# Kernel optimization log

Measured on AMD Instinct MI355X. Metric: run time of the kernel, lower is better.

## Reference

```python
import jax, jax.numpy as jnp
import numpy as np

B, N, D, K = 4, 256, 128, 8
H = 2 * D   # MLP hidden
F3 = 3 * D  # pair feature dim


def setup_inputs() -> dict:
    key = jax.random.key(0)
    ks = jax.random.split(key, 9)
    init = lambda k, shape: (jax.random.normal(k, shape, jnp.float32) * 0.02)
    s = jax.random.normal(ks[0], (B, N, D), jnp.float32)
    return {
        "s": s,
        "Wg1": init(ks[1], (F3, H)), "bg1": jnp.zeros((H,), jnp.float32),
        "Wg2": init(ks[2], (H, 1)),  "bg2": jnp.zeros((1,), jnp.float32),
        "Wa1": init(ks[3], (F3, H)), "ba1": jnp.zeros((H,), jnp.float32),
        "Wa2": init(ks[4], (H, 1)),  "ba2": jnp.zeros((1,), jnp.float32),
    }


def _mlp(x, W1, b1, W2, b2):
    # 2-layer MLP: Linear -> ReLU -> Linear (dropout inactive at eval)
    return jax.nn.relu(x @ W1 + b1) @ W2 + b2


def reference(s, Wg1, bg1, Wg2, bg2, Wa1, ba1, Wa2, ba2):
    b, n, d = s.shape
    si = s[:, :, None, :]                      # [B,N,1,D]
    sj = s[:, None, :, :]                      # [B,1,N,D]
    pair = jnp.concatenate([
        jnp.broadcast_to(si, (b, n, n, d)),
        jnp.broadcast_to(sj, (b, n, n, d)),
        si * sj,
    ], axis=-1)                                # [B,N,N,3D]

    # Stage 1: discrete top-K peer gating
    scores = _mlp(pair, Wg1, bg1, Wg2, bg2)[..., 0]   # [B,N,N]
    k = min(K, n)
    _, topk_idx = jax.lax.top_k(scores, k)            # [B,N,K]
    gate = jax.nn.one_hot(topk_idx, n, dtype=jnp.float32).sum(-2)  # [B,N,N] binary

    # Stage 2: soft relevance weighting over selected peers
    att_logits = _mlp(pair, Wa1, ba1, Wa2, ba2)[..., 0]            # [B,N,N]
    att_logits = jnp.where(gate > 0, att_logits, -jnp.inf)
    att_weights = jnp.nan_to_num(jax.nn.softmax(att_logits, axis=-1))

    ctx = jnp.einsum('bij,bij,bjd->bid', gate, att_weights, s)     # [B,N,D]
    return ctx, gate, att_weights
```

## Files before the change

kernel.cpp:

```cpp
#include <hip/hip_runtime.h>
#include <math.h>

#define B_ 4
#define N_ 256
#define D_ 128
#define H_ 256
#define K_ 8
#define NJP 64

typedef short v8s __attribute__((ext_vector_type(8)));
typedef float v16f __attribute__((ext_vector_type(16)));

__device__ inline void split_bf16(float x, unsigned short& hi, unsigned short& lo) {
  unsigned u = __float_as_uint(x);
  unsigned uh = u & 0xFFFF0000u;
  hi = (unsigned short)(uh >> 16);
  float r = x - __uint_as_float(uh);
  unsigned ur = __float_as_uint(r);
  ur += 0x7FFFu + ((ur >> 16) & 1u);
  lo = (unsigned short)(ur >> 16);
}

__global__ __launch_bounds__(256) void prep_all(
    const float* __restrict__ s,
    const float* __restrict__ Wg1, const float* __restrict__ bg1,
    const float* __restrict__ Wa1, const float* __restrict__ ba1,
    float* __restrict__ Ag, float* __restrict__ Aa,
    unsigned short* __restrict__ Wghi, unsigned short* __restrict__ Wglo,
    unsigned short* __restrict__ Wahi,
    unsigned short* __restrict__ Sfh, unsigned short* __restrict__ Sfl) {
  __shared__ float sh[D_];
  const int blk = blockIdx.x;
  if (blk < 1024) {
    const int b = blk >> 8, n = blk & 255, h = threadIdx.x;
    if (h < D_) sh[h] = s[(b * N_ + n) * D_ + h];
    __syncthreads();
    float ag = bg1[h], aa = ba1[h];
#pragma unroll 8
    for (int d = 0; d < D_; d++) {
      ag = fmaf(sh[d], Wg1[d * H_ + h], ag);
      aa = fmaf(sh[d], Wa1[d * H_ + h], aa);
    }
    Ag[(b * N_ + n) * H_ + h] = ag;
    Aa[(b * N_ + n) * H_ + h] = aa;
  } else if (blk < 1152) {
    const int id = blk - 1024;
    if (threadIdx.x < 64) {
      const int ks = id >> 3, tile = id & 7, lane = threadIdx.x;
      const int h = tile * 32 + (lane & 31);
      const int kbase = ks * 16 + (lane >> 5) * 8;
      const int idx0 = (id * 64 + lane) * 8;
#pragma unroll
      for (int e = 0; e < 8; e++) {
        const int k = kbase + e;
        const int f = (k < D_) ? (2 * D_ + k) : k;
        unsigned short x, y;
        split_bf16(Wg1[f * H_ + h], x, y);
        Wghi[idx0 + e] = x;
        Wglo[idx0 + e] = y;
        unsigned short xa, ya;
        split_bf16(Wa1[f * H_ + h], xa, ya);
        Wahi[idx0 + e] = xa;
      }
    }
  } else {
    const int id = blk - 1152;
    const int b = id >> 3, jt = id & 7;
    const int lane = threadIdx.x & 63, k0 = threadIdx.x >> 6;
    const int j = jt * 32 + (lane & 31);
#pragma unroll
    for (int ksl = k0; ksl < 8; ksl += 4) {
      const int d = ksl * 16 + (lane >> 5) * 8;
      const float* sp = s + (b * N_ + j) * D_ + d;
      const float4 f0 = *(const float4*)(sp);
      const float4 f1 = *(const float4*)(sp + 4);
      v8s vh, vl;
      unsigned short x, y;
      split_bf16(f0.x, x, y); vh[0] = (short)x; vl[0] = (short)y;
      split_bf16(f0.y, x, y); vh[1] = (short)x; vl[1] = (short)y;
      split_bf16(f0.z, x, y); vh[2] = (short)x; vl[2] = (short)y;
      split_bf16(f0.w, x, y); vh[3] = (short)x; vl[3] = (short)y;
      split_bf16(f1.x, x, y); vh[4] = (short)x; vl[4] = (short)y;
      split_bf16(f1.y, x, y); vh[5] = (short)x; vl[5] = (short)y;
      split_bf16(f1.z, x, y); vh[6] = (short)x; vl[6] = (short)y;
      split_bf16(f1.w, x, y); vh[7] = (short)x; vl[7] = (short)y;
      const int dst = (((b * 8 + jt) * 8 + ksl) * 64 + lane) * 8;
      *(v8s*)(Sfh + dst) = vh;
      *(v8s*)(Sfl + dst) = vl;
    }
  }
}

__device__ inline void arg_better(float v2, int i2, float& v, int& idx) {
  if (v2 > v || (v2 == v && i2 < idx)) { v = v2; idx = i2; }
}

__device__ inline int a_idx(int jl, int k) {
  return (((jl >> 5) * 8 + (k >> 4)) * 64 + ((k >> 3) & 1) * 32 + (jl & 31)) * 8
         + (k & 7);
}
#define ALO 8192

__global__ __launch_bounds__(256, 2) void score_kernel(
    const float* __restrict__ s,
    const float* __restrict__ Ag, const float* __restrict__ Aa,
    const unsigned short* __restrict__ Sfh, const unsigned short* __restrict__ Sfl,
    const unsigned short* __restrict__ Wghi, const unsigned short* __restrict__ Wglo,
    const unsigned short* __restrict__ Wahi,
    const float* __restrict__ Wg2, const float* __restrict__ bg2p,
    const float* __restrict__ Wa2, const float* __restrict__ ba2p,
    float* __restrict__ out) {
  const int b = blockIdx.x >> 8;
  const int i = blockIdx.x & 255;
  const int t = threadIdx.x;
  const int wv = t >> 6, lane = t & 63;
  const int m32 = lane & 31, half32 = lane >> 5;

  __shared__ __align__(16) unsigned short a_all[2 * ALO + 64];
  __shared__ float si_sh[D_];
  __shared__ float sc_part[8 * NJP];
  __shared__ float scg_sh[N_];
  __shared__ float attl_sh[N_];
  __shared__ float red_v[4];
  __shared__ int red_i[4];
  __shared__ int sel_list[K_];

  if (t < D_) si_sh[t] = s[(b * N_ + i) * D_ + t];

  float agv[2], w2g[2], aav[2], w2a[2];
#pragma unroll
  for (int ht = 0; ht < 2; ht++) {
    const int hg = wv * 64 + ht * 32 + m32;
    agv[ht] = Ag[(b * N_ + i) * H_ + hg];
    w2g[ht] = Wg2[hg];
    aav[ht] = Aa[(b * N_ + i) * H_ + hg];
    w2a[ht] = Wa2[hg];
  }

  const int boff = ((2 * wv) * 64 + lane) * 8;

#define MF(A_, B_v, C_) C_ = __builtin_amdgcn_mfma_f32_32x32x16_bf16(A_, B_v, C_, 0, 0, 0)

#pragma unroll 1
  for (int ph = 0; ph < 4; ph++) {
    __syncthreads();
    {
      const int jl = t >> 2, kq = t & 3;
      const int jg = b * N_ + ph * NJP + jl;
      const float* srow = s + jg * D_ + kq * 32;
      const float* sic = si_sh + kq * 32;
#pragma unroll
      for (int u = 0; u < 4; u++) {
        const float4 sv0 = *(const float4*)(srow + u * 8);
        const float4 sv1 = *(const float4*)(srow + u * 8 + 4);
        v8s vh, vl;
        unsigned short x, y;
        split_bf16(sic[u * 8 + 0] * sv0.x, x, y); vh[0] = (short)x; vl[0] = (short)y;
        split_bf16(sic[u * 8 + 1] * sv0.y, x, y); vh[1] = (short)x; vl[1] = (short)y;
        split_bf16(sic[u * 8 + 2] * sv0.z, x, y); vh[2] = (short)x; vl[2] = (short)y;
        split_bf16(sic[u * 8 + 3] * sv0.w, x, y); vh[3] = (short)x; vl[3] = (short)y;
        split_bf16(sic[u * 8 + 4] * sv1.x, x, y); vh[4] = (short)x; vl[4] = (short)y;
        split_bf16(sic[u * 8 + 5] * sv1.y, x, y); vh[5] = (short)x; vl[5] = (short)y;
        split_bf16(sic[u * 8 + 6] * sv1.z, x, y); vh[6] = (short)x; vl[6] = (short)y;
        split_bf16(sic[u * 8 + 7] * sv1.w, x, y); vh[7] = (short)x; vl[7] = (short)y;
        const int idx = a_idx(jl, kq * 32 + u * 8);
        *(v8s*)(a_all + idx) = vh;
        *(v8s*)(a_all + ALO + idx) = vl;
      }
    }
    __syncthreads();

    const unsigned short* sf_base_h = Sfh + ((b * 8 + ph * 2) * 8) * 512 + lane * 8;
    const unsigned short* sf_base_l = Sfl + ((b * 8 + ph * 2) * 8) * 512 + lane * 8;

    v16f g00, g01, g10, g11, a00, a01, a10, a11;
    g00 = g01 = g10 = g11 = (v16f)(0.f);
    a00 = a01 = a10 = a11 = (v16f)(0.f);

    {
      const unsigned short* pgh = Wghi + boff;
      const unsigned short* pgl = Wglo + boff;
      const unsigned short* pah = Wahi + boff;
      v8s bh[2][2], bl[2][2], ba[2][2];
      bh[0][0] = *(const v8s*)pgh;  bh[0][1] = *(const v8s*)(pgh + 512);
      bl[0][0] = *(const v8s*)pgl;  bl[0][1] = *(const v8s*)(pgl + 512);
      ba[0][0] = *(const v8s*)pah;  ba[0][1] = *(const v8s*)(pah + 512);
      pgh += 4096;  pgl += 4096;  pah += 4096;

      const unsigned short* ahp = a_all + lane * 8;
#pragma unroll 2
      for (int ks = 0; ks < 8; ks++) {
        const int cur = ks & 1, nxt = cur ^ 1;
        bh[nxt][0] = *(const v8s*)pgh;  bh[nxt][1] = *(const v8s*)(pgh + 512);
        bl[nxt][0] = *(const v8s*)pgl;  bl[nxt][1] = *(const v8s*)(pgl + 512);
        ba[nxt][0] = *(const v8s*)pah;  ba[nxt][1] = *(const v8s*)(pah + 512);
        pgh += 4096;  pgl += 4096;  pah += 4096;
        v8s ah0 = *(const v8s*)(ahp);
        v8s ah1 = *(const v8s*)(ahp + 4096);
        v8s al0 = *(const v8s*)(ahp + ALO);
        v8s al1 = *(const v8s*)(ahp + ALO + 4096);
        ahp += 512;
        MF(ah0, bh[cur][0], g00); MF(ah0, bh[cur][1], g01);
        MF(ah0, ba[cur][0], a00); MF(ah0, ba[cur][1], a01);
        MF(ah0, bl[cur][0], g00); MF(ah0, bl[cur][1], g01);
        MF(al0, bh[cur][0], g00); MF(al0, bh[cur][1], g01);
        MF(ah1, bh[cur][0], g10); MF(ah1, bh[cur][1], g11);
        MF(ah1, ba[cur][0], a10); MF(ah1, ba[cur][1], a11);
        MF(ah1, bl[cur][0], g10); MF(ah1, bl[cur][1], g11);
        MF(al1, bh[cur][0], g10); MF(al1, bh[cur][1], g11);
      }
      const unsigned short* sfh = sf_base_h;
      const unsigned short* sfl = sf_base_l;
#pragma unroll 2
      for (int ks = 8; ks < 16; ks++) {
        const int cur = ks & 1, nxt = cur ^ 1;
        bh[nxt][0] = *(const v8s*)pgh;  bh[nxt][1] = *(const v8s*)(pgh + 512);
        bl[nxt][0] = *(const v8s*)pgl;  bl[nxt][1] = *(const v8s*)(pgl + 512);
        ba[nxt][0] = *(const v8s*)pah;  ba[nxt][1] = *(const v8s*)(pah + 512);
        pgh += 4096;  pgl += 4096;  pah += 4096;
        v8s ah0 = *(const v8s*)(sfh);
        v8s ah1 = *(const v8s*)(sfh + 4096);
        v8s al0 = *(const v8s*)(sfl);
        v8s al1 = *(const v8s*)(sfl + 4096);
        sfh += 512;  sfl += 512;
        MF(ah0, bh[cur][0], g00); MF(ah0, bh[cur][1], g01);
        MF(ah0, ba[cur][0], a00); MF(ah0, ba[cur][1], a01);
        MF(ah0, bl[cur][0], g00); MF(ah0, bl[cur][1], g01);
        MF(al0, bh[cur][0], g00); MF(al0, bh[cur][1], g01);
        MF(ah1, bh[cur][0], g10); MF(ah1, bh[cur][1], g11);
        MF(ah1, ba[cur][0], a10); MF(ah1, ba[cur][1], a11);
        MF(ah1, bl[cur][0], g10); MF(ah1, bl[cur][1], g11);
        MF(al1, bh[cur][0], g10); MF(al1, bh[cur][1], g11);
      }
    }

    {
      float sg[32];
#pragma unroll
      for (int m = 0; m < 32; m++) sg[m] = 0.f;
#pragma unroll
      for (int r = 0; r < 16; r++) {
        sg[r]      = fmaf(fmaxf(g00[r] + agv[0], 0.f), w2g[0], sg[r]);
        sg[r]      = fmaf(fmaxf(g01[r] + agv[1], 0.f), w2g[1], sg[r]);
        sg[16 + r] = fmaf(fmaxf(g10[r] + agv[0], 0.f), w2g[0], sg[16 + r]);
        sg[16 + r] = fmaf(fmaxf(g11[r] + agv[1], 0.f), w2g[1], sg[16 + r]);
      }
#pragma unroll
      for (int m = 0; m < 32; m++) {
        float v = sg[m];
#pragma unroll
        for (int off = 1; off <= 16; off <<= 1) v += __shfl_xor(v, off, 64);
        sg[m] = v;
      }
      if (m32 == 0) {
#pragma unroll
        for (int jt = 0; jt < 2; jt++)
#pragma unroll
          for (int r = 0; r < 16; r++) {
            const int jl = jt * 32 + (r & 3) + 8 * (r >> 2) + 4 * half32;
            sc_part[wv * NJP + jl] = sg[jt * 16 + r];
          }
      }
      float sa[32];
#pragma unroll
      for (int m = 0; m < 32; m++) sa[m] = 0.f;
#pragma unroll
      for (int r = 0; r < 16; r++) {
        sa[r]      = fmaf(fmaxf(a00[r] + aav[0], 0.f), w2a[0], sa[r]);
        sa[r]      = fmaf(fmaxf(a01[r] + aav[1], 0.f), w2a[1], sa[r]);
        sa[16 + r] = fmaf(fmaxf(a10[r] + aav[0], 0.f), w2a[0], sa[16 + r]);
        sa[16 + r] = fmaf(fmaxf(a11[r] + aav[1], 0.f), w2a[1], sa[16 + r]);
      }
#pragma unroll
      for (int m = 0; m < 32; m++) {
        float v = sa[m];
#pragma unroll
        for (int off = 1; off <= 16; off <<= 1) v += __shfl_xor(v, off, 64);
        sa[m] = v;
      }
      if (m32 == 0) {
#pragma unroll
        for (int jt = 0; jt < 2; jt++)
#pragma unroll
          for (int r = 0; r < 16; r++) {
            const int jl = jt * 32 + (r & 3) + 8 * (r >> 2) + 4 * half32;
            sc_part[4 * NJP + wv * NJP + jl] = sa[jt * 16 + r];
          }
      }
    }
    __syncthreads();
    if (t < NJP) {
      scg_sh[ph * NJP + t] = sc_part[t] + sc_part[NJP + t] + sc_part[2 * NJP + t]
                           + sc_part[3 * NJP + t] + bg2p[0];
      attl_sh[ph * NJP + t] = sc_part[4 * NJP + t] + sc_part[5 * NJP + t]
                            + sc_part[6 * NJP + t] + sc_part[7 * NJP + t] + ba2p[0];
    }
  }
  __syncthreads();

  for (int k = 0; k < K_; k++) {
    float v = scg_sh[t];
    int idx = t;
#pragma unroll
    for (int off = 32; off > 0; off >>= 1) {
      const float vo = __shfl_down(v, off, 64);
      const int io = __shfl_down(idx, off, 64);
      arg_better(vo, io, v, idx);
    }
    if ((t & 63) == 0) { red_v[t >> 6] = v; red_i[t >> 6] = idx; }
    __syncthreads();
    if (t == 0) {
      float bv = red_v[0];
      int bi = red_i[0];
      for (int w = 1; w < 4; w++) arg_better(red_v[w], red_i[w], bv, bi);
      sel_list[k] = bi;
      scg_sh[bi] = -INFINITY;
    }
    __syncthreads();
  }

  bool selj = false;
#pragma unroll
  for (int k = 0; k < K_; k++) selj = selj || (sel_list[k] == t);

  if (t == 0) {
    float m = -INFINITY;
    for (int k = 0; k < K_; k++) m = fmaxf(m, attl_sh[sel_list[k]]);
    float ssum = 0.f;
    for (int k = 0; k < K_; k++) ssum += expf(attl_sh[sel_list[k]] - m);
    red_v[0] = m;
    red_v[1] = ssum;
  }
  __syncthreads();
  const float att = selj ? expf(attl_sh[t] - red_v[0]) / red_v[1] : 0.f;

  float* __restrict__ ctx_out = out;
  float* __restrict__ gate_out = out + B_ * N_ * D_;
  float* __restrict__ att_out = out + B_ * N_ * D_ + B_ * N_ * N_;

  const int row = (b * N_ + i) * N_;
  gate_out[row + t] = selj ? 1.f : 0.f;
  att_out[row + t] = att;

  __syncthreads();
  attl_sh[t] = att;
  __syncthreads();

  if (t < D_) {
    float acc2 = 0.f;
#pragma unroll
    for (int k = 0; k < K_; k++) {
      const int jj = sel_list[k];
      acc2 = fmaf(attl_sh[jj], s[(b * N_ + jj) * D_ + t], acc2);
    }
    ctx_out[(b * N_ + i) * D_ + t] = acc2;
  }
#undef MF
}

extern "C" void kernel_launch(void* const* d_in, const int* in_sizes, int n_in,
                              void* d_out, int out_size, void* d_ws, size_t ws_size,
                              hipStream_t stream) {
  const float* s   = (const float*)d_in[0];
  const float* Wg1 = (const float*)d_in[1];
  const float* bg1 = (const float*)d_in[2];
  const float* Wg2 = (const float*)d_in[3];
  const float* bg2 = (const float*)d_in[4];
  const float* Wa1 = (const float*)d_in[5];
  const float* ba1 = (const float*)d_in[6];
  const float* Wa2 = (const float*)d_in[7];
  const float* ba2 = (const float*)d_in[8];
  float* out = (float*)d_out;

  float* ws = (float*)d_ws;
  float* Ag = ws;
  float* Aa = Ag + B_ * N_ * H_;
  unsigned short* Wghi = (unsigned short*)(Aa + B_ * N_ * H_);
  unsigned short* Wglo = Wghi + 65536 + 4096;
  unsigned short* Wahi = Wglo + 65536 + 4096;
  unsigned short* Sfh  = Wahi + 65536 + 4096;
  unsigned short* Sfl  = Sfh + B_ * 32768;

  prep_all<<<dim3(1184), dim3(256), 0, stream>>>(
      s, Wg1, bg1, Wa1, ba1, Ag, Aa, Wghi, Wglo, Wahi, Sfh, Sfl);
  score_kernel<<<dim3(B_ * N_), dim3(256), 0, stream>>>(
      s, Ag, Aa, Sfh, Sfl, Wghi, Wglo, Wahi, Wg2, bg2, Wa2, ba2, out);
}
```

Baseline: 241.4 us.

## Double j-tile per phase and split gate/attention MFMA passes

Each phase now covers 128 peer columns instead of 64, halving the phase count and the syncs and B-fragment loads per peer. To keep accumulator register pressure manageable, the gating and attention MLP products are computed in two separate sequential passes over the shared A tile, each holding eight 32x32 accumulators. The reduction now spreads the gate and attention sums across all 256 threads. This doubles LDS use for the A tile, which may reduce occupancy, and the larger accumulator sets raise VGPR pressure.

```diff
diff --git a/kernel.cpp b/kernel.cpp
--- a/kernel.cpp
+++ b/kernel.cpp
@@ -6,7 +6,7 @@
 #define D_ 128
 #define H_ 256
 #define K_ 8
-#define NJP 64
+#define NJP 128
 
 typedef short v8s __attribute__((ext_vector_type(8)));
 typedef float v16f __attribute__((ext_vector_type(16)));
@@ -99,7 +99,7 @@
   return (((jl >> 5) * 8 + (k >> 4)) * 64 + ((k >> 3) & 1) * 32 + (jl & 31)) * 8
          + (k & 7);
 }
-#define ALO 8192
+#define ALO 16384
 
 __global__ __launch_bounds__(256, 2) void score_kernel(
     const float* __restrict__ s,
@@ -118,7 +118,7 @@
 
   __shared__ __align__(16) unsigned short a_all[2 * ALO + 64];
   __shared__ float si_sh[D_];
-  __shared__ float sc_part[8 * NJP];
+  __shared__ float sc_part[2 * 4 * NJP];
   __shared__ float scg_sh[N_];
   __shared__ float attl_sh[N_];
   __shared__ float red_v[4];
@@ -142,15 +142,15 @@
 #define MF(A_, B_v, C_) C_ = __builtin_amdgcn_mfma_f32_32x32x16_bf16(A_, B_v, C_, 0, 0, 0)
 
 #pragma unroll 1
-  for (int ph = 0; ph < 4; ph++) {
+  for (int ph = 0; ph < 2; ph++) {
     __syncthreads();
     {
-      const int jl = t >> 2, kq = t & 3;
+      const int jl = t >> 1, kq = t & 1;
       const int jg = b * N_ + ph * NJP + jl;
-      const float* srow = s + jg * D_ + kq * 32;
-      const float* sic = si_sh + kq * 32;
-#pragma unroll
-      for (int u = 0; u < 4; u++) {
+      const float* srow = s + jg * D_ + kq * 64;
+      const float* sic = si_sh + kq * 64;
+#pragma unroll
+      for (int u = 0; u < 8; u++) {
         const float4 sv0 = *(const float4*)(srow + u * 8);
         const float4 sv1 = *(const float4*)(srow + u * 8 + 4);
         v8s vh, vl;
@@ -163,29 +163,29 @@
         split_bf16(sic[u * 8 + 5] * sv1.y, x, y); vh[5] = (short)x; vl[5] = (short)y;
         split_bf16(sic[u * 8 + 6] * sv1.z, x, y); vh[6] = (short)x; vl[6] = (short)y;
         split_bf16(sic[u * 8 + 7] * sv1.w, x, y); vh[7] = (short)x; vl[7] = (short)y;
-        const int idx = a_idx(jl, kq * 32 + u * 8);
+        const int idx = a_idx(jl, kq * 64 + u * 8);
         *(v8s*)(a_all + idx) = vh;
         *(v8s*)(a_all + ALO + idx) = vl;
       }
     }
     __syncthreads();
 
-    const unsigned short* sf_base_h = Sfh + ((b * 8 + ph * 2) * 8) * 512 + lane * 8;
-    const unsigned short* sf_base_l = Sfl + ((b * 8 + ph * 2) * 8) * 512 + lane * 8;
-
-    v16f g00, g01, g10, g11, a00, a01, a10, a11;
-    g00 = g01 = g10 = g11 = (v16f)(0.f);
-    a00 = a01 = a10 = a11 = (v16f)(0.f);
+    const unsigned short* sf_h = Sfh + ((b * 8 + ph * 4) * 8) * 512 + lane * 8;
+    const unsigned short* sf_l = Sfl + ((b * 8 + ph * 4) * 8) * 512 + lane * 8;
 
     {
+      v16f g[4][2];
+#pragma unroll
+      for (int jt = 0; jt < 4; jt++)
+#pragma unroll
+        for (int ht = 0; ht < 2; ht++) g[jt][ht] = (v16f)(0.f);
+
       const unsigned short* pgh = Wghi + boff;
       const unsigned short* pgl = Wglo + boff;
-      const unsigned short* pah = Wahi + boff;
-      v8s bh[2][2], bl[2][2], ba[2][2];
+      v8s bh[2][2], bl[2][2];
       bh[0][0] = *(const v8s*)pgh;  bh[0][1] = *(const v8s*)(pgh + 512);
       bl[0][0] = *(const v8s*)pgl;  bl[0][1] = *(const v8s*)(pgl + 512);
-      ba[0][0] = *(const v8s*)pah;  ba[0][1] = *(const v8s*)(pah + 512);
-      pgh += 4096;  pgl += 4096;  pah += 4096;
+      pgh += 4096;  pgl += 4096;
 
       const unsigned short* ahp = a_all + lane * 8;
 #pragma unroll 2
@@ -193,94 +193,146 @@
         const int cur = ks & 1, nxt = cur ^ 1;
         bh[nxt][0] = *(const v8s*)pgh;  bh[nxt][1] = *(const v8s*)(pgh + 512);
         bl[nxt][0] = *(const v8s*)pgl;  bl[nxt][1] = *(const v8s*)(pgl + 512);
-        ba[nxt][0] = *(const v8s*)pah;  ba[nxt][1] = *(const v8s*)(pah + 512);
-        pgh += 4096;  pgl += 4096;  pah += 4096;
+        pgh += 4096;  pgl += 4096;
         v8s ah0 = *(const v8s*)(ahp);
         v8s ah1 = *(const v8s*)(ahp + 4096);
+        v8s ah2 = *(const v8s*)(ahp + 8192);
+        v8s ah3 = *(const v8s*)(ahp + 12288);
         v8s al0 = *(const v8s*)(ahp + ALO);
         v8s al1 = *(const v8s*)(ahp + ALO + 4096);
+        v8s al2 = *(const v8s*)(ahp + ALO + 8192);
+        v8s al3 = *(const v8s*)(ahp + ALO + 12288);
         ahp += 512;
-        MF(ah0, bh[cur][0], g00); MF(ah0, bh[cur][1], g01);
-        MF(ah0, ba[cur][0], a00); MF(ah0, ba[cur][1], a01);
-        MF(ah0, bl[cur][0], g00); MF(ah0, bl[cur][1], g01);
-        MF(al0, bh[cur][0], g00); MF(al0, bh[cur][1], g01);
-        MF(ah1, bh[cur][0], g10); MF(ah1, bh[cur][1], g11);
-        MF(ah1, ba[cur][0], a10); MF(ah1, ba[cur][1], a11);
-        MF(ah1, bl[cur][0], g10); MF(ah1, bl[cur][1], g11);
-        MF(al1, bh[cur][0], g10); MF(al1, bh[cur][1], g11);
-      }
-      const unsigned short* sfh = sf_base_h;
-      const unsigned short* sfl = sf_base_l;
+        MF(ah0, bh[cur][0], g[0][0]); MF(ah0, bh[cur][1], g[0][1]);
+        MF(ah0, bl[cur][0], g[0][0]); MF(ah0, bl[cur][1], g[0][1]);
+        MF(al0, bh[cur][0], g[0][0]); MF(al0, bh[cur][1], g[0][1]);
+        MF(ah1, bh[cur][0], g[1][0]); MF(ah1, bh[cur][1], g[1][1]);
+        MF(ah1, bl[cur][0], g[1][0]); MF(ah1, bl[cur][1], g[1][1]);
+        MF(al1, bh[cur][0], g[1][0]); MF(al1, bh[cur][1], g[1][1]);
+        MF(ah2, bh[cur][0], g[2][0]); MF(ah2, bh[cur][1], g[2][1]);
+        MF(ah2, bl[cur][0], g[2][0]); MF(ah2, bl[cur][1], g[2][1]);
+        MF(al2, bh[cur][0], g[2][0]); MF(al2, bh[cur][1], g[2][1]);
+        MF(ah3, bh[cur][0], g[3][0]); MF(ah3, bh[cur][1], g[3][1]);
+        MF(ah3, bl[cur][0], g[3][0]); MF(ah3, bl[cur][1], g[3][1]);
+        MF(al3, bh[cur][0], g[3][0]); MF(al3, bh[cur][1], g[3][1]);
+      }
+      const unsigned short* sh0 = sf_h;
+      const unsigned short* sh1 = sf_h + 4096;
+      const unsigned short* sh2 = sf_h + 8192;
+      const unsigned short* sh3 = sf_h + 12288;
+      const unsigned short* sl0 = sf_l;
+      const unsigned short* sl1 = sf_l + 4096;
+      const unsigned short* sl2 = sf_l + 8192;
+      const unsigned short* sl3 = sf_l + 12288;
 #pragma unroll 2
       for (int ks = 8; ks < 16; ks++) {
         const int cur = ks & 1, nxt = cur ^ 1;
         bh[nxt][0] = *(const v8s*)pgh;  bh[nxt][1] = *(const v8s*)(pgh + 512);
         bl[nxt][0] = *(const v8s*)pgl;  bl[nxt][1] = *(const v8s*)(pgl + 512);
-        ba[nxt][0] = *(const v8s*)pah;  ba[nxt][1] = *(const v8s*)(pah + 512);
-        pgh += 4096;  pgl += 4096;  pah += 4096;
-        v8s ah0 = *(const v8s*)(sfh);
-        v8s ah1 = *(const v8s*)(sfh + 4096);
-        v8s al0 = *(const v8s*)(sfl);
-        v8s al1 = *(const v8s*)(sfl + 4096);
-        sfh += 512;  sfl += 512;
-        MF(ah0, bh[cur][0], g00); MF(ah0, bh[cur][1], g01);
-        MF(ah0, ba[cur][0], a00); MF(ah0, ba[cur][1], a01);
-        MF(ah0, bl[cur][0], g00); MF(ah0, bl[cur][1], g01);
-        MF(al0, bh[cur][0], g00); MF(al0, bh[cur][1], g01);
-        MF(ah1, bh[cur][0], g10); MF(ah1, bh[cur][1], g11);
-        MF(ah1, ba[cur][0], a10); MF(ah1, ba[cur][1], a11);
-        MF(ah1, bl[cur][0], g10); MF(ah1, bl[cur][1], g11);
-        MF(al1, bh[cur][0], g10); MF(al1, bh[cur][1], g11);
-      }
-    }
-
-    {
-      float sg[32];
-#pragma unroll
-      for (int m = 0; m < 32; m++) sg[m] = 0.f;
-#pragma unroll
-      for (int r = 0; r < 16; r++) {
-        sg[r]      = fmaf(fmaxf(g00[r] + agv[0], 0.f), w2g[0], sg[r]);
-        sg[r]      = fmaf(fmaxf(g01[r] + agv[1], 0.f), w2g[1], sg[r]);
-        sg[16 + r] = fmaf(fmaxf(g10[r] + agv[0], 0.f), w2g[0], sg[16 + r]);
-        sg[16 + r] = fmaf(fmaxf(g11[r] + agv[1], 0.f), w2g[1], sg[16 + r]);
-      }
-#pragma unroll
-      for (int m = 0; m < 32; m++) {
-        float v = sg[m];
-#pragma unroll
-        for (int off = 1; off <= 16; off <<= 1) v += __shfl_xor(v, off, 64);
-        sg[m] = v;
-      }
+        pgh += 4096;  pgl += 4096;
+        v8s ah0 = *(const v8s*)sh0;  sh0 += 512;
+        v8s ah1 = *(const v8s*)sh1;  sh1 += 512;
+        v8s ah2 = *(const v8s*)sh2;  sh2 += 512;
+        v8s ah3 = *(const v8s*)sh3;  sh3 += 512;
+        v8s al0 = *(const v8s*)sl0;  sl0 += 512;
+        v8s al1 = *(const v8s*)sl1;  sl1 += 512;
+        v8s al2 = *(const v8s*)sl2;  sl2 += 512;
+        v8s al3 = *(const v8s*)sl3;  sl3 += 512;
+        MF(ah0, bh[cur][0], g[0][0]); MF(ah0, bh[cur][1], g[0][1]);
+        MF(ah0, bl[cur][0], g[0][0]); MF(ah0, bl[cur][1], g[0][1]);
+        MF(al0, bh[cur][0], g[0][0]); MF(al0, bh[cur][1], g[0][1]);
+        MF(ah1, bh[cur][0], g[1][0]); MF(ah1, bh[cur][1], g[1][1]);
+        MF(ah1, bl[cur][0], g[1][0]); MF(ah1, bl[cur][1], g[1][1]);
+        MF(al1, bh[cur][0], g[1][0]); MF(al1, bh[cur][1], g[1][1]);
+        MF(ah2, bh[cur][0], g[2][0]); MF(ah2, bh[cur][1], g[2][1]);
+        MF(ah2, bl[cur][0], g[2][0]); MF(ah2, bl[cur][1], g[2][1]);
+        MF(al2, bh[cur][0], g[2][0]); MF(al2, bh[cur][1], g[2][1]);
+        MF(ah3, bh[cur][0], g[3][0]); MF(ah3, bh[cur][1], g[3][1]);
+        MF(ah3, bl[cur][0], g[3][0]); MF(ah3, bl[cur][1], g[3][1]);
+        MF(al3, bh[cur][0], g[3][0]); MF(al3, bh[cur][1], g[3][1]);
+      }
+      float sg[64];
+#pragma unroll
+      for (int jt = 0; jt < 4; jt++)
+#pragma unroll
+        for (int r = 0; r < 16; r++) {
+          float v = fmaxf(g[jt][0][r] + agv[0], 0.f) * w2g[0]
+                  + fmaxf(g[jt][1][r] + agv[1], 0.f) * w2g[1];
+#pragma unroll
+          for (int off = 1; off <= 16; off <<= 1) v += __shfl_xor(v, off, 64);
+          sg[jt * 16 + r] = v;
+        }
       if (m32 == 0) {
 #pragma unroll
-        for (int jt = 0; jt < 2; jt++)
+        for (int jt = 0; jt < 4; jt++)
 #pragma unroll
           for (int r = 0; r < 16; r++) {
             const int jl = jt * 32 + (r & 3) + 8 * (r >> 2) + 4 * half32;
             sc_part[wv * NJP + jl] = sg[jt * 16 + r];
           }
       }
-      float sa[32];
-#pragma unroll
-      for (int m = 0; m < 32; m++) sa[m] = 0.f;
-#pragma unroll
-      for (int r = 0; r < 16; r++) {
-        sa[r]      = fmaf(fmaxf(a00[r] + aav[0], 0.f), w2a[0], sa[r]);
-        sa[r]      = fmaf(fmaxf(a01[r] + aav[1], 0.f), w2a[1], sa[r]);
-        sa[16 + r] = fmaf(fmaxf(a10[r] + aav[0], 0.f), w2a[0], sa[16 + r]);
-        sa[16 + r] = fmaf(fmaxf(a11[r] + aav[1], 0.f), w2a[1], sa[16 + r]);
-      }
-#pragma unroll
-      for (int m = 0; m < 32; m++) {
-        float v = sa[m];
-#pragma unroll
-        for (int off = 1; off <= 16; off <<= 1) v += __shfl_xor(v, off, 64);
-        sa[m] = v;
-      }
+    }
+
+    {
+      v16f a[4][2];
+#pragma unroll
+      for (int jt = 0; jt < 4; jt++)
+#pragma unroll
+        for (int ht = 0; ht < 2; ht++) a[jt][ht] = (v16f)(0.f);
+
+      const unsigned short* pah = Wahi + boff;
+      v8s ba[2][2];
+      ba[0][0] = *(const v8s*)pah;  ba[0][1] = *(const v8s*)(pah + 512);
+      pah += 4096;
+
+      const unsigned short* ahp = a_all + lane * 8;
+#pragma unroll 2
+      for (int ks = 0; ks < 8; ks++) {
+        const int cur = ks & 1, nxt = cur ^ 1;
+        ba[nxt][0] = *(const v8s*)pah;  ba[nxt][1] = *(const v8s*)(pah + 512);
+        pah += 4096;
+        v8s ah0 = *(const v8s*)(ahp);
+        v8s ah1 = *(const v8s*)(ahp + 4096);
+        v8s ah2 = *(const v8s*)(ahp + 8192);
+        v8s ah3 = *(const v8s*)(ahp + 12288);
+        ahp += 512;
+        MF(ah0, ba[cur][0], a[0][0]); MF(ah0, ba[cur][1], a[0][1]);
+        MF(ah1, ba[cur][0], a[1][0]); MF(ah1, ba[cur][1], a[1][1]);
+        MF(ah2, ba[cur][0], a[2][0]); MF(ah2, ba[cur][1], a[2][1]);
+        MF(ah3, ba[cur][0], a[3][0]); MF(ah3, ba[cur][1], a[3][1]);
+      }
+      const unsigned short* sh0 = sf_h;
+      const unsigned short* sh1 = sf_h + 4096;
+      const unsigned short* sh2 = sf_h + 8192;
+      const unsigned short* sh3 = sf_h + 12288;
+#pragma unroll 2
+      for (int ks = 8; ks < 16; ks++) {
+        const int cur = ks & 1, nxt = cur ^ 1;
+        ba[nxt][0] = *(const v8s*)pah;  ba[nxt][1] = *(const v8s*)(pah + 512);
+        pah += 4096;
+        v8s ah0 = *(const v8s*)sh0;  sh0 += 512;
+        v8s ah1 = *(const v8s*)sh1;  sh1 += 512;
+        v8s ah2 = *(const v8s*)sh2;  sh2 += 512;
+        v8s ah3 = *(const v8s*)sh3;  sh3 += 512;
+        MF(ah0, ba[cur][0], a[0][0]); MF(ah0, ba[cur][1], a[0][1]);
+        MF(ah1, ba[cur][0], a[1][0]); MF(ah1, ba[cur][1], a[1][1]);
+        MF(ah2, ba[cur][0], a[2][0]); MF(ah2, ba[cur][1], a[2][1]);
+        MF(ah3, ba[cur][0], a[3][0]); MF(ah3, ba[cur][1], a[3][1]);
+      }
+      float sa[64];
+#pragma unroll
+      for (int jt = 0; jt < 4; jt++)
+#pragma unroll
+        for (int r = 0; r < 16; r++) {
+          float v = fmaxf(a[jt][0][r] + aav[0], 0.f) * w2a[0]
+                  + fmaxf(a[jt][1][r] + aav[1], 0.f) * w2a[1];
+#pragma unroll
+          for (int off = 1; off <= 16; off <<= 1) v += __shfl_xor(v, off, 64);
+          sa[jt * 16 + r] = v;
+        }
       if (m32 == 0) {
 #pragma unroll
-        for (int jt = 0; jt < 2; jt++)
+        for (int jt = 0; jt < 4; jt++)
 #pragma unroll
           for (int r = 0; r < 16; r++) {
             const int jl = jt * 32 + (r & 3) + 8 * (r >> 2) + 4 * half32;
@@ -292,8 +344,10 @@
     if (t < NJP) {
       scg_sh[ph * NJP + t] = sc_part[t] + sc_part[NJP + t] + sc_part[2 * NJP + t]
                            + sc_part[3 * NJP + t] + bg2p[0];
-      attl_sh[ph * NJP + t] = sc_part[4 * NJP + t] + sc_part[5 * NJP + t]
-                            + sc_part[6 * NJP + t] + sc_part[7 * NJP + t] + ba2p[0];
+    } else {
+      const int jl = t - NJP;
+      attl_sh[ph * NJP + jl] = sc_part[4 * NJP + jl] + sc_part[5 * NJP + jl]
+                             + sc_part[6 * NJP + jl] + sc_part[7 * NJP + jl] + ba2p[0];
     }
   }
   __syncthreads();
```

Result: no change. 243.9 us (+1.0%).
